# Performance work log

Hardware: AMD Instinct MI355X
Metric: run time of the kernel (lower is better)

The kernel has to match this reference:

```python
import jax, jax.numpy as jnp
import numpy as np

N_NODES = 50000
N_EDGES = 800000
F_IN = 128
HID = 64
N_LAYERS = 3
N_GRAPHS = 64
N_CLASS = 2


def setup_inputs() -> dict:
    key = jax.random.key(0)
    ks = jax.random.split(key, 8)
    x = jax.random.normal(ks[0], (N_NODES, F_IN), jnp.float32)
    edge_index = jax.random.randint(ks[1], (2, N_EDGES), 0, N_NODES, dtype=jnp.int32)
    # sorted, balanced graph assignment so every graph id appears (max-pool safe)
    batch = (jnp.arange(N_NODES, dtype=jnp.int32) * N_GRAPHS) // N_NODES

    def lin(k, fi, fo):
        return jax.random.normal(k, (fi, fo), jnp.float32) / np.sqrt(fi).astype(np.float32)

    W1 = lin(ks[2], F_IN, HID)
    W2 = lin(ks[3], HID, HID)
    W3 = lin(ks[4], HID, HID)
    lin1_W = lin(ks[5], 3 * N_LAYERS * HID, HID)
    lin2_W = lin(ks[6], HID, N_CLASS)
    return dict(
        x=x,
        W1=W1, b1=jnp.zeros((HID,), jnp.float32),
        W2=W2, b2=jnp.zeros((HID,), jnp.float32),
        W3=W3, b3=jnp.zeros((HID,), jnp.float32),
        lin1_W=lin1_W, lin1_b=jnp.zeros((HID,), jnp.float32),
        lin2_W=lin2_W, lin2_b=jnp.zeros((N_CLASS,), jnp.float32),
        edge_index=edge_index, batch=batch,
    )


def reference(x, W1, b1, W2, b2, W3, b3, lin1_W, lin1_b, lin2_W, lin2_b,
              edge_index, batch):
    src, dst = edge_index[0], edge_index[1]
    # GCN symmetric normalization with self-loops (computed once, shared by layers)
    deg = jax.ops.segment_sum(jnp.ones((N_EDGES,), jnp.float32), dst, N_NODES) + 1.0
    dinv = jax.lax.rsqrt(deg)                      # [N]
    enorm = dinv[src] * dinv[dst]                  # [E]
    self_norm = (dinv * dinv)[:, None]             # [N,1] self-loop coeff

    def gcn_conv(h, W, b):
        h = h @ W                                  # [N, HID]
        agg = jax.ops.segment_sum(h[src] * enorm[:, None], dst, N_NODES)
        return agg + self_norm * h + b

    h = jax.nn.relu(gcn_conv(x, W1, b1))
    xs = [h]
    for W, b in ((W2, b2), (W3, b3)):
        h = jax.nn.relu(gcn_conv(h, W, b))
        xs.append(h)
    hcat = jnp.concatenate(xs, axis=1)             # JK 'cat': [N, 3*HID]

    add = jax.ops.segment_sum(hcat, batch, N_GRAPHS)
    cnt = jax.ops.segment_sum(jnp.ones((N_NODES,), jnp.float32), batch, N_GRAPHS)
    mean = add / cnt[:, None]
    mx = jax.ops.segment_max(hcat, batch, N_GRAPHS)
    g = jnp.concatenate([add, mean, mx], axis=1)   # [G, 9*HID]

    g = jax.nn.relu(g @ lin1_W + lin1_b)
    # dropout p=0.5 is identity in eval mode
    logits = g @ lin2_W + lin2_b
    return jax.nn.log_softmax(logits, axis=-1)
```

## Files before the change

### kernel.cpp

```cpp
#include <hip/hip_runtime.h>
#include <hip/hip_fp16.h>

#define N_NODES 50000
#define N_EDGES 800000
#define F_IN 128
#define HID 64
#define N_GRAPHS 64

#define SCAN_B ((N_NODES + 255) / 256)
#define FUSE_B ((N_EDGES + 255) / 256)

typedef _Float16 half8 __attribute__((ext_vector_type(8)));
typedef float f32x4 __attribute__((ext_vector_type(4)));

__global__ void deg_pack(const int* __restrict__ ei, int* __restrict__ ideg, int E,
                         const float* __restrict__ W1, const float* __restrict__ W2,
                         const float* __restrict__ W3,
                         __half* __restrict__ W1t, __half* __restrict__ W2t,
                         __half* __restrict__ W3t) {
    int i = blockIdx.x * blockDim.x + threadIdx.x;
    if (i * 4 < E) {
        int4 d = ((const int4*)(ei + E))[i];
        atomicAdd(&ideg[d.x], 1);
        atomicAdd(&ideg[d.y], 1);
        atomicAdd(&ideg[d.z], 1);
        atomicAdd(&ideg[d.w], 1);
    }
    if (i < 8192) {
        int f = i >> 7, k = i & 127;
        W1t[i] = __float2half(W1[k * 64 + f]);
    } else if (i < 12288) {
        int j = i - 8192;
        int f = j >> 6, k = j & 63;
        W2t[j] = __float2half(W2[k * 64 + f]);
    } else if (i < 16384) {
        int l = i - 12288;
        int f = l >> 6, k = l & 63;
        W3t[l] = __float2half(W3[k * 64 + f]);
    }
}

__global__ void scan_part(const int* __restrict__ ideg, int* __restrict__ bsum,
                          float* __restrict__ padd, unsigned int* __restrict__ pmax,
                          int* __restrict__ pcnt, int n) {
    __shared__ int s[256];
    int t = threadIdx.x;
    if (blockIdx.x < 48) {
        int z = blockIdx.x * 256 + t;
        padd[z] = 0.f;
        pmax[z] = 0u;
        if (z < 64) pcnt[z] = 0;
    }
    int i = blockIdx.x * 256 + t;
    s[t] = (i < n) ? ideg[i] : 0;
    __syncthreads();
    for (int o = 128; o > 0; o >>= 1) {
        if (t < o) s[t] += s[t + o];
        __syncthreads();
    }
    if (t == 0) bsum[blockIdx.x] = s[0];
}

__global__ void scan_final(const int* __restrict__ ideg, const int* __restrict__ bsum,
                           int* __restrict__ offs, int* __restrict__ cur,
                           float* __restrict__ dinv, int n) {
    __shared__ int s[256];
    __shared__ int sb[256];
    int t = threadIdx.x;
    int i = blockIdx.x * 256 + t;
    int v = (i < n) ? ideg[i] : 0;
    s[t] = v;
    sb[t] = (t < SCAN_B) ? bsum[t] : 0;
    __syncthreads();
    for (int o = 1; o < 256; o <<= 1) {
        int u  = (t >= o) ? s[t - o] : 0;
        int ub = (t >= o) ? sb[t - o] : 0;
        __syncthreads();
        s[t] += u; sb[t] += ub;
        __syncthreads();
    }
    int base = (blockIdx.x == 0) ? 0 : sb[blockIdx.x - 1];
    int excl = base + s[t] - v;
    if (i < n) {
        offs[i] = excl; cur[i] = excl;
        dinv[i] = rsqrtf((float)v + 1.0f);
    }
    if (i == n - 1) offs[n] = excl + v;
}

__global__ __launch_bounds__(256) void fused_fill_mm1(
        const int* __restrict__ ei, const float* __restrict__ dinv,
        int* __restrict__ cur, unsigned int* __restrict__ csr,
        const float* __restrict__ X, const __half* __restrict__ W1t,
        __half* __restrict__ Y16, int E) {
    constexpr int SX = 136;
    __shared__ __half sXh[16 * SX];
    int tid = threadIdx.x;

    int e = blockIdx.x * 256 + tid;
    int esrc = ei[e];
    int d = ei[E + e];
    __half hw = __float2half(dinv[esrc]);
    unsigned int pk = ((unsigned int)(*(unsigned short*)&hw) << 16)
                    | (unsigned int)(esrc & 0xFFFF);
    int pos = atomicAdd(&cur[d], 1);

    int lane = tid & 63;
    int r = lane & 15, h = lane >> 4;
    int w = tid >> 6;
    const half8* Brow = (const half8*)(W1t + (size_t)(w * 16 + r) * F_IN + h * 8);
    half8 b0 = Brow[0];
    half8 b1 = Brow[4];
    half8 b2 = Brow[8];
    half8 b3 = Brow[12];

    int nodeBase = blockIdx.x * 16;
#pragma unroll
    for (int p = tid; p < 512; p += 256) {
        int row = p >> 5, c4 = p & 31;
        float4 v = *(const float4*)(X + (size_t)(nodeBase + row) * F_IN + c4 * 4);
        __half2 ab = __floats2half2_rn(v.x, v.y);
        __half2 cd = __floats2half2_rn(v.z, v.w);
        uint2 u; u.x = *(unsigned int*)&ab; u.y = *(unsigned int*)&cd;
        *(uint2*)&sXh[row * SX + c4 * 4] = u;
    }
    __syncthreads();

    f32x4 acc = {0.f, 0.f, 0.f, 0.f};
    half8 a0 = *(const half8*)&sXh[r * SX +  0 + h * 8];
    half8 a1 = *(const half8*)&sXh[r * SX + 32 + h * 8];
    half8 a2 = *(const half8*)&sXh[r * SX + 64 + h * 8];
    half8 a3 = *(const half8*)&sXh[r * SX + 96 + h * 8];
    acc = __builtin_amdgcn_mfma_f32_16x16x32_f16(a0, b0, acc, 0, 0, 0);
    acc = __builtin_amdgcn_mfma_f32_16x16x32_f16(a1, b1, acc, 0, 0, 0);
    acc = __builtin_amdgcn_mfma_f32_16x16x32_f16(a2, b2, acc, 0, 0, 0);
    acc = __builtin_amdgcn_mfma_f32_16x16x32_f16(a3, b3, acc, 0, 0, 0);
    int nodeT = nodeBase + h * 4;
#pragma unroll
    for (int reg = 0; reg < 4; ++reg)
        Y16[(size_t)(nodeT + reg) * 64 + w * 16 + r] = __float2half(acc[reg]);

    csr[pos] = pk;
}

__global__ __launch_bounds__(256) void matmul64_h(
        const __half* __restrict__ X, const __half* __restrict__ Wt,
        __half* __restrict__ Y16, int n) {
    int tid = threadIdx.x;
    int nodeBase = blockIdx.x * 64;
    int lane = tid & 63;
    int r = lane & 15, h = lane >> 4;
    int w = tid >> 6;
    int rowA = nodeBase + w * 16 + r;
    const half8* Arow = (const half8*)(X + (size_t)rowA * 64 + h * 8);
    half8 a0 = Arow[0];
    half8 a1 = Arow[4];
#pragma unroll
    for (int ft = 0; ft < 4; ++ft) {
        const half8* Brow = (const half8*)(Wt + (size_t)(ft * 16 + r) * 64 + h * 8);
        half8 b0 = Brow[0];
        half8 b1 = Brow[4];
        f32x4 acc = {0.f, 0.f, 0.f, 0.f};
        acc = __builtin_amdgcn_mfma_f32_16x16x32_f16(a0, b0, acc, 0, 0, 0);
        acc = __builtin_amdgcn_mfma_f32_16x16x32_f16(a1, b1, acc, 0, 0, 0);
        int nodeT = nodeBase + w * 16 + h * 4;
#pragma unroll
        for (int reg = 0; reg < 4; ++reg) {
            int node = nodeT + reg;
            if (node < n) Y16[(size_t)node * 64 + ft * 16 + r] = __float2half(acc[reg]);
        }
    }
}

__global__ void agg_kernel(const __half* __restrict__ hp16, const float* __restrict__ dinv,
                           const int* __restrict__ offs, const unsigned int* __restrict__ csr,
                           const float* __restrict__ b, __half* __restrict__ hout, int n) {
    int node = blockIdx.x * 4 + (threadIdx.x >> 6);
    if (node >= n) return;
    int lane = threadIdx.x & 63;
    int g = lane >> 3;
    int sub = lane & 7;
    int beg = offs[node], end = offs[node + 1];

    float dn = dinv[node];
    uint4 sv = *(const uint4*)(hp16 + (size_t)node * 64 + sub * 8);
    float4 bA = *(const float4*)(b + sub * 8);
    float4 bB = *(const float4*)(b + sub * 8 + 4);

    float a0 = 0.f, a1 = 0.f, a2 = 0.f, a3 = 0.f;
    float a4 = 0.f, a5 = 0.f, a6 = 0.f, a7 = 0.f;
    int lim = end - 1;
#pragma unroll 1
    for (int base0 = beg; base0 < end; base0 += 32) {
        int base = base0 + g * 4;
        if (base < end) {
            unsigned int pk0 = csr[base];
            unsigned int pk1 = csr[min(base + 1, lim)];
            unsigned int pk2 = csr[min(base + 2, lim)];
            unsigned int pk3 = csr[min(base + 3, lim)];
            uint4 hv0 = *(const uint4*)(hp16 + (size_t)(pk0 & 0xFFFFu) * 64 + sub * 8);
            uint4 hv1 = *(const uint4*)(hp16 + (size_t)(pk1 & 0xFFFFu) * 64 + sub * 8);
            uint4 hv2 = *(const uint4*)(hp16 + (size_t)(pk2 & 0xFFFFu) * 64 + sub * 8);
            uint4 hv3 = *(const uint4*)(hp16 + (size_t)(pk3 & 0xFFFFu) * 64 + sub * 8);
#pragma unroll
            for (int j = 0; j < 4; ++j) {
                unsigned int pkj = (j == 0) ? pk0 : (j == 1) ? pk1 : (j == 2) ? pk2 : pk3;
                uint4 hvj = (j == 0) ? hv0 : (j == 1) ? hv1 : (j == 2) ? hv2 : hv3;
                __half_raw hr; hr.x = (unsigned short)(pkj >> 16);
                float w = (base + j < end) ? __half2float(*(__half*)&hr) : 0.f;
                float2 f01 = __half22float2(*(const __half2*)&hvj.x);
                float2 f23 = __half22float2(*(const __half2*)&hvj.y);
                float2 f45 = __half22float2(*(const __half2*)&hvj.z);
                float2 f67 = __half22float2(*(const __half2*)&hvj.w);
                a0 += f01.x * w; a1 += f01.y * w; a2 += f23.x * w; a3 += f23.y * w;
                a4 += f45.x * w; a5 += f45.y * w; a6 += f67.x * w; a7 += f67.y * w;
            }
        }
    }
#pragma unroll
    for (int m = 8; m <= 32; m <<= 1) {
        a0 += __shfl_xor(a0, m); a1 += __shfl_xor(a1, m);
        a2 += __shfl_xor(a2, m); a3 += __shfl_xor(a3, m);
        a4 += __shfl_xor(a4, m); a5 += __shfl_xor(a5, m);
        a6 += __shfl_xor(a6, m); a7 += __shfl_xor(a7, m);
    }

    float2 s01 = __half22float2(*(const __half2*)&sv.x);
    float2 s23 = __half22float2(*(const __half2*)&sv.y);
    float2 s45 = __half22float2(*(const __half2*)&sv.z);
    float2 s67 = __half22float2(*(const __half2*)&sv.w);
    float dn2 = dn * dn;
    float4 rA, rB;
    rA.x = dn * a0 + dn2 * s01.x + bA.x;  rA.x = rA.x > 0.f ? rA.x : 0.f;
    rA.y = dn * a1 + dn2 * s01.y + bA.y;  rA.y = rA.y > 0.f ? rA.y : 0.f;
    rA.z = dn * a2 + dn2 * s23.x + bA.z;  rA.z = rA.z > 0.f ? rA.z : 0.f;
    rA.w = dn * a3 + dn2 * s23.y + bA.w;  rA.w = rA.w > 0.f ? rA.w : 0.f;
    rB.x = dn * a4 + dn2 * s45.x + bB.x;  rB.x = rB.x > 0.f ? rB.x : 0.f;
    rB.y = dn * a5 + dn2 * s45.y + bB.y;  rB.y = rB.y > 0.f ? rB.y : 0.f;
    rB.z = dn * a6 + dn2 * s67.x + bB.z;  rB.z = rB.z > 0.f ? rB.z : 0.f;
    rB.w = dn * a7 + dn2 * s67.y + bB.w;  rB.w = rB.w > 0.f ? rB.w : 0.f;
    if (g == 0) {
        __half2 p0 = __floats2half2_rn(rA.x, rA.y);
        __half2 p1 = __floats2half2_rn(rA.z, rA.w);
        __half2 p2 = __floats2half2_rn(rB.x, rB.y);
        __half2 p3 = __floats2half2_rn(rB.z, rB.w);
        uint4 st;
        st.x = *(unsigned int*)&p0; st.y = *(unsigned int*)&p1;
        st.z = *(unsigned int*)&p2; st.w = *(unsigned int*)&p3;
        *(uint4*)(hout + (size_t)node * 64 + sub * 8) = st;
    }
}

__global__ __launch_bounds__(192) void pool_kernel(
        const __half* __restrict__ h1, const __half* __restrict__ h2,
        const __half* __restrict__ h3, const int* __restrict__ batch,
        float* __restrict__ padd, unsigned int* __restrict__ pmax,
        int* __restrict__ pcnt, int n, int chunk) {
    __shared__ float lsum[8][192];
    __shared__ float lmax[8][192];
    int t = threadIdx.x;
    int stream = t / 24;
    int oct = t % 24;
    int L = oct >> 3, sub = oct & 7;
    int f0 = L * 64 + sub * 8;
    const __half* src = (L == 0) ? h1 : (L == 1) ? h2 : h3;
    int start = blockIdx.x * chunk;
    int end = min(start + chunk, n);
    if (start >= end) return;
    int gtail = batch[end - 1];

    float s[8] = {0.f,0.f,0.f,0.f,0.f,0.f,0.f,0.f};
    float m[8] = {0.f,0.f,0.f,0.f,0.f,0.f,0.f,0.f};
    int cnt = 0;
    int node = start + stream;
    int gcur = (node < end) ? batch[node] : gtail;
    for (; node < end; node += 8) {
        int bg = batch[node];
        if (bg != gcur) {
#pragma unroll
            for (int j = 0; j < 8; ++j) {
                unsafeAtomicAdd(&padd[gcur * 192 + f0 + j], s[j]);
                atomicMax(&pmax[gcur * 192 + f0 + j], __float_as_uint(m[j]));
                s[j] = 0.f; m[j] = 0.f;
            }
            if (oct == 0) { atomicAdd(&pcnt[gcur], cnt); cnt = 0; }
            gcur = bg;
        }
        uint4 hv = *(const uint4*)(src + (size_t)node * 64 + sub * 8);
        const __half2* hp = (const __half2*)&hv;
#pragma unroll
        for (int q = 0; q < 4; ++q) {
            float2 f2 = __half22float2(hp[q]);
            s[2*q]   += f2.x;  m[2*q]   = fmaxf(m[2*q],   f2.x);
            s[2*q+1] += f2.y;  m[2*q+1] = fmaxf(m[2*q+1], f2.y);
        }
        if (oct == 0) ++cnt;
    }
    if (oct == 0 && cnt) atomicAdd(&pcnt[gcur], cnt);
    if (gcur != gtail) {
#pragma unroll
        for (int j = 0; j < 8; ++j) {
            unsafeAtomicAdd(&padd[gcur * 192 + f0 + j], s[j]);
            atomicMax(&pmax[gcur * 192 + f0 + j], __float_as_uint(m[j]));
            s[j] = 0.f; m[j] = 0.f;
        }
    }
#pragma unroll
    for (int j = 0; j < 8; ++j) {
        lsum[stream][f0 + j] = s[j];
        lmax[stream][f0 + j] = m[j];
    }
    __syncthreads();
    float ts = 0.f, tm = 0.f;
#pragma unroll
    for (int st = 0; st < 8; ++st) {
        ts += lsum[st][t];
        tm = fmaxf(tm, lmax[st][t]);
    }
    unsafeAtomicAdd(&padd[gtail * 192 + t], ts);
    atomicMax(&pmax[gtail * 192 + t], __float_as_uint(tm));
}

__global__ void mlp_kernel(const float* __restrict__ padd, const unsigned int* __restrict__ pmax,
                           const int* __restrict__ pcnt,
                           const float* __restrict__ lin1_W, const float* __restrict__ lin1_b,
                           const float* __restrict__ lin2_W, const float* __restrict__ lin2_b,
                           float* __restrict__ out) {
    int g = blockIdx.x;
    int t = threadIdx.x;
    __shared__ float gv[576];
    __shared__ float hid[64];
    float cnt = (float)pcnt[g];
    for (int i = t; i < 192; i += 64) {
        float a = padd[g * 192 + i];
        gv[i] = a;
        gv[192 + i] = a / cnt;
        gv[384 + i] = __uint_as_float(pmax[g * 192 + i]);
    }
    __syncthreads();
    float acc = lin1_b[t];
#pragma unroll 8
    for (int k = 0; k < 576; ++k) acc += gv[k] * lin1_W[k * 64 + t];
    hid[t] = acc > 0.0f ? acc : 0.0f;
    __syncthreads();
    if (t == 0) {
        float l0 = lin2_b[0], l1 = lin2_b[1];
        for (int k = 0; k < 64; ++k) {
            l0 += hid[k] * lin2_W[k * 2 + 0];
            l1 += hid[k] * lin2_W[k * 2 + 1];
        }
        float m = fmaxf(l0, l1);
        float lse = m + logf(expf(l0 - m) + expf(l1 - m));
        out[g * 2 + 0] = l0 - lse;
        out[g * 2 + 1] = l1 - lse;
    }
}

extern "C" void kernel_launch(void* const* d_in, const int* in_sizes, int n_in,
                              void* d_out, int out_size, void* d_ws, size_t ws_size,
                              hipStream_t stream) {
    const float* x      = (const float*)d_in[0];
    const float* W1     = (const float*)d_in[1];
    const float* b1     = (const float*)d_in[2];
    const float* W2     = (const float*)d_in[3];
    const float* b2     = (const float*)d_in[4];
    const float* W3     = (const float*)d_in[5];
    const float* b3     = (const float*)d_in[6];
    const float* lin1_W = (const float*)d_in[7];
    const float* lin1_b = (const float*)d_in[8];
    const float* lin2_W = (const float*)d_in[9];
    const float* lin2_b = (const float*)d_in[10];
    const int*   ei     = (const int*)d_in[11];
    const int*   batch  = (const int*)d_in[12];
    float* out = (float*)d_out;

    char* ws = (char*)d_ws;
    size_t off = 0;
    auto alloc = [&](size_t bytes) {
        void* p = ws + off;
        off = (off + bytes + 255) & ~(size_t)255;
        return p;
    };
    int*   ideg    = (int*)  alloc(N_NODES * 4);
    float* dinv    = (float*)alloc(N_NODES * 4);
    int*   offs    = (int*)  alloc((N_NODES + 1) * 4);
    int*   cur     = (int*)  alloc(N_NODES * 4);
    int*   bsum    = (int*)  alloc(SCAN_B * 4);
    unsigned int* csr = (unsigned int*)alloc((size_t)N_EDGES * 4);
    __half* P      = (__half*)alloc((size_t)N_NODES * 64 * 2);
    __half* h1     = (__half*)alloc((size_t)N_NODES * 64 * 2);
    __half* h2     = (__half*)alloc((size_t)N_NODES * 64 * 2);
    __half* h3     = (__half*)alloc((size_t)N_NODES * 64 * 2);
    __half* W1t    = (__half*)alloc(64 * 128 * 2);
    __half* W2t    = (__half*)alloc(64 * 64 * 2);
    __half* W3t    = (__half*)alloc(64 * 64 * 2);
    float* padd    = (float*)alloc(N_GRAPHS * 192 * 4);
    unsigned int* pmax = (unsigned int*)alloc(N_GRAPHS * 192 * 4);
    int*   pcnt    = (int*) alloc(N_GRAPHS * 4);

    hipMemsetAsync(ideg, 0, N_NODES * 4, stream);
    deg_pack<<<(N_EDGES / 4 + 255) / 256, 256, 0, stream>>>(ei, ideg, N_EDGES,
                                                            W1, W2, W3, W1t, W2t, W3t);
    scan_part <<<SCAN_B, 256, 0, stream>>>(ideg, bsum, padd, pmax, pcnt, N_NODES);
    scan_final<<<SCAN_B, 256, 0, stream>>>(ideg, bsum, offs, cur, dinv, N_NODES);

    const int mmGrid  = (N_NODES + 63) / 64;
    const int aggGrid = (N_NODES + 3) / 4;

    fused_fill_mm1<<<FUSE_B, 256, 0, stream>>>(ei, dinv, cur, csr, x, W1t, P, N_EDGES);
    agg_kernel<<<aggGrid, 256, 0, stream>>>(P, dinv, offs, csr, b1, h1, N_NODES);
    matmul64_h<<<mmGrid, 256, 0, stream>>>(h1, W2t, P, N_NODES);
    agg_kernel<<<aggGrid, 256, 0, stream>>>(P, dinv, offs, csr, b2, h2, N_NODES);
    matmul64_h<<<mmGrid, 256, 0, stream>>>(h2, W3t, P, N_NODES);
    agg_kernel<<<aggGrid, 256, 0, stream>>>(P, dinv, offs, csr, b3, h3, N_NODES);

    const int chunk = (N_NODES + 511) / 512;
    pool_kernel<<<512, 192, 0, stream>>>(h1, h2, h3, batch, padd, pmax, pcnt, N_NODES, chunk);
    mlp_kernel<<<N_GRAPHS, 64, 0, stream>>>(padd, pmax, pcnt, lin1_W, lin1_b, lin2_W, lin2_b, out);
}
```

Measured before the change: 319.2 us.

## Fold source-side normalization into matmul output and shrink CSR to 16-bit indices

Each matmul epilogue now scales its output rows by dinv, so the aggregation sums unweighted neighbour rows. The per-edge weight no longer has to be stored in the CSR, which shrinks to 16-bit source indices and halves the index traffic read in each of the three aggregation passes. It also drops the dinv gather in the fill kernel. The self-loop term becomes dn*(agg+self), which is algebraically equivalent. The fp16 intermediate is now pre-scaled, which slightly changes rounding. The matmul reads dinv as float4 past N_NODES in its last block, and the 16-bit index truncation was already present.

```diff
diff --git a/kernel.cpp b/kernel.cpp
--- a/kernel.cpp
+++ b/kernel.cpp
@@ -90,7 +90,7 @@
 
 __global__ __launch_bounds__(256) void fused_fill_mm1(
         const int* __restrict__ ei, const float* __restrict__ dinv,
-        int* __restrict__ cur, unsigned int* __restrict__ csr,
+        int* __restrict__ cur, unsigned short* __restrict__ csr,
         const float* __restrict__ X, const __half* __restrict__ W1t,
         __half* __restrict__ Y16, int E) {
     constexpr int SX = 136;
@@ -98,11 +98,8 @@
     int tid = threadIdx.x;
 
     int e = blockIdx.x * 256 + tid;
-    int esrc = ei[e];
+    unsigned short srcu = (unsigned short)(ei[e] & 0xFFFF);
     int d = ei[E + e];
-    __half hw = __float2half(dinv[esrc]);
-    unsigned int pk = ((unsigned int)(*(unsigned short*)&hw) << 16)
-                    | (unsigned int)(esrc & 0xFFFF);
     int pos = atomicAdd(&cur[d], 1);
 
     int lane = tid & 63;
@@ -136,16 +133,18 @@
     acc = __builtin_amdgcn_mfma_f32_16x16x32_f16(a2, b2, acc, 0, 0, 0);
     acc = __builtin_amdgcn_mfma_f32_16x16x32_f16(a3, b3, acc, 0, 0, 0);
     int nodeT = nodeBase + h * 4;
+    float4 dv = *(const float4*)(dinv + nodeT);
+    acc[0] *= dv.x; acc[1] *= dv.y; acc[2] *= dv.z; acc[3] *= dv.w;
 #pragma unroll
     for (int reg = 0; reg < 4; ++reg)
         Y16[(size_t)(nodeT + reg) * 64 + w * 16 + r] = __float2half(acc[reg]);
 
-    csr[pos] = pk;
+    csr[pos] = srcu;
 }
 
 __global__ __launch_bounds__(256) void matmul64_h(
         const __half* __restrict__ X, const __half* __restrict__ Wt,
-        __half* __restrict__ Y16, int n) {
+        const float* __restrict__ dinv, __half* __restrict__ Y16, int n) {
     int tid = threadIdx.x;
     int nodeBase = blockIdx.x * 64;
     int lane = tid & 63;
@@ -155,6 +154,8 @@
     const half8* Arow = (const half8*)(X + (size_t)rowA * 64 + h * 8);
     half8 a0 = Arow[0];
     half8 a1 = Arow[4];
+    int nodeT = nodeBase + w * 16 + h * 4;
+    float4 dv = *(const float4*)(dinv + nodeT);
 #pragma unroll
     for (int ft = 0; ft < 4; ++ft) {
         const half8* Brow = (const half8*)(Wt + (size_t)(ft * 16 + r) * 64 + h * 8);
@@ -163,7 +164,7 @@
         f32x4 acc = {0.f, 0.f, 0.f, 0.f};
         acc = __builtin_amdgcn_mfma_f32_16x16x32_f16(a0, b0, acc, 0, 0, 0);
         acc = __builtin_amdgcn_mfma_f32_16x16x32_f16(a1, b1, acc, 0, 0, 0);
-        int nodeT = nodeBase + w * 16 + h * 4;
+        acc[0] *= dv.x; acc[1] *= dv.y; acc[2] *= dv.z; acc[3] *= dv.w;
 #pragma unroll
         for (int reg = 0; reg < 4; ++reg) {
             int node = nodeT + reg;
@@ -173,7 +174,7 @@
 }
 
 __global__ void agg_kernel(const __half* __restrict__ hp16, const float* __restrict__ dinv,
-                           const int* __restrict__ offs, const unsigned int* __restrict__ csr,
+                           const int* __restrict__ offs, const unsigned short* __restrict__ csr,
                            const float* __restrict__ b, __half* __restrict__ hout, int n) {
     int node = blockIdx.x * 4 + (threadIdx.x >> 6);
     if (node >= n) return;
@@ -194,20 +195,16 @@
     for (int base0 = beg; base0 < end; base0 += 32) {
         int base = base0 + g * 4;
         if (base < end) {
-            unsigned int pk0 = csr[base];
-            unsigned int pk1 = csr[min(base + 1, lim)];
-            unsigned int pk2 = csr[min(base + 2, lim)];
-            unsigned int pk3 = csr[min(base + 3, lim)];
-            uint4 hv0 = *(const uint4*)(hp16 + (size_t)(pk0 & 0xFFFFu) * 64 + sub * 8);
-            uint4 hv1 = *(const uint4*)(hp16 + (size_t)(pk1 & 0xFFFFu) * 64 + sub * 8);
-            uint4 hv2 = *(const uint4*)(hp16 + (size_t)(pk2 & 0xFFFFu) * 64 + sub * 8);
-            uint4 hv3 = *(const uint4*)(hp16 + (size_t)(pk3 & 0xFFFFu) * 64 + sub * 8);
+            int i0 = base, i1 = min(base + 1, lim), i2 = min(base + 2, lim), i3 = min(base + 3, lim);
+            unsigned short s0 = csr[i0], s1 = csr[i1], s2 = csr[i2], s3 = csr[i3];
+            uint4 hv0 = *(const uint4*)(hp16 + (size_t)s0 * 64 + sub * 8);
+            uint4 hv1 = *(const uint4*)(hp16 + (size_t)s1 * 64 + sub * 8);
+            uint4 hv2 = *(const uint4*)(hp16 + (size_t)s2 * 64 + sub * 8);
+            uint4 hv3 = *(const uint4*)(hp16 + (size_t)s3 * 64 + sub * 8);
 #pragma unroll
             for (int j = 0; j < 4; ++j) {
-                unsigned int pkj = (j == 0) ? pk0 : (j == 1) ? pk1 : (j == 2) ? pk2 : pk3;
                 uint4 hvj = (j == 0) ? hv0 : (j == 1) ? hv1 : (j == 2) ? hv2 : hv3;
-                __half_raw hr; hr.x = (unsigned short)(pkj >> 16);
-                float w = (base + j < end) ? __half2float(*(__half*)&hr) : 0.f;
+                float w = (base + j < end) ? 1.f : 0.f;
                 float2 f01 = __half22float2(*(const __half2*)&hvj.x);
                 float2 f23 = __half22float2(*(const __half2*)&hvj.y);
                 float2 f45 = __half22float2(*(const __half2*)&hvj.z);
@@ -229,16 +226,15 @@
     float2 s23 = __half22float2(*(const __half2*)&sv.y);
     float2 s45 = __half22float2(*(const __half2*)&sv.z);
     float2 s67 = __half22float2(*(const __half2*)&sv.w);
-    float dn2 = dn * dn;
     float4 rA, rB;
-    rA.x = dn * a0 + dn2 * s01.x + bA.x;  rA.x = rA.x > 0.f ? rA.x : 0.f;
-    rA.y = dn * a1 + dn2 * s01.y + bA.y;  rA.y = rA.y > 0.f ? rA.y : 0.f;
-    rA.z = dn * a2 + dn2 * s23.x + bA.z;  rA.z = rA.z > 0.f ? rA.z : 0.f;
-    rA.w = dn * a3 + dn2 * s23.y + bA.w;  rA.w = rA.w > 0.f ? rA.w : 0.f;
-    rB.x = dn * a4 + dn2 * s45.x + bB.x;  rB.x = rB.x > 0.f ? rB.x : 0.f;
-    rB.y = dn * a5 + dn2 * s45.y + bB.y;  rB.y = rB.y > 0.f ? rB.y : 0.f;
-    rB.z = dn * a6 + dn2 * s67.x + bB.z;  rB.z = rB.z > 0.f ? rB.z : 0.f;
-    rB.w = dn * a7 + dn2 * s67.y + bB.w;  rB.w = rB.w > 0.f ? rB.w : 0.f;
+    rA.x = dn * (a0 + s01.x) + bA.x;  rA.x = rA.x > 0.f ? rA.x : 0.f;
+    rA.y = dn * (a1 + s01.y) + bA.y;  rA.y = rA.y > 0.f ? rA.y : 0.f;
+    rA.z = dn * (a2 + s23.x) + bA.z;  rA.z = rA.z > 0.f ? rA.z : 0.f;
+    rA.w = dn * (a3 + s23.y) + bA.w;  rA.w = rA.w > 0.f ? rA.w : 0.f;
+    rB.x = dn * (a4 + s45.x) + bB.x;  rB.x = rB.x > 0.f ? rB.x : 0.f;
+    rB.y = dn * (a5 + s45.y) + bB.y;  rB.y = rB.y > 0.f ? rB.y : 0.f;
+    rB.z = dn * (a6 + s67.x) + bB.z;  rB.z = rB.z > 0.f ? rB.z : 0.f;
+    rB.w = dn * (a7 + s67.y) + bB.w;  rB.w = rB.w > 0.f ? rB.w : 0.f;
     if (g == 0) {
         __half2 p0 = __floats2half2_rn(rA.x, rA.y);
         __half2 p1 = __floats2half2_rn(rA.z, rA.w);
@@ -386,7 +382,7 @@
     int*   offs    = (int*)  alloc((N_NODES + 1) * 4);
     int*   cur     = (int*)  alloc(N_NODES * 4);
     int*   bsum    = (int*)  alloc(SCAN_B * 4);
-    unsigned int* csr = (unsigned int*)alloc((size_t)N_EDGES * 4);
+    unsigned short* csr = (unsigned short*)alloc((size_t)N_EDGES * 2);
     __half* P      = (__half*)alloc((size_t)N_NODES * 64 * 2);
     __half* h1     = (__half*)alloc((size_t)N_NODES * 64 * 2);
     __half* h2     = (__half*)alloc((size_t)N_NODES * 64 * 2);
@@ -409,9 +405,9 @@
 
     fused_fill_mm1<<<FUSE_B, 256, 0, stream>>>(ei, dinv, cur, csr, x, W1t, P, N_EDGES);
     agg_kernel<<<aggGrid, 256, 0, stream>>>(P, dinv, offs, csr, b1, h1, N_NODES);
-    matmul64_h<<<mmGrid, 256, 0, stream>>>(h1, W2t, P, N_NODES);
+    matmul64_h<<<mmGrid, 256, 0, stream>>>(h1, W2t, dinv, P, N_NODES);
     agg_kernel<<<aggGrid, 256, 0, stream>>>(P, dinv, offs, csr, b2, h2, N_NODES);
-    matmul64_h<<<mmGrid, 256, 0, stream>>>(h2, W3t, P, N_NODES);
+    matmul64_h<<<mmGrid, 256, 0, stream>>>(h2, W3t, dinv, P, N_NODES);
     agg_kernel<<<aggGrid, 256, 0, stream>>>(P, dinv, offs, csr, b3, h3, N_NODES);
 
     const int chunk = (N_NODES + 511) / 512;
```

After: 319.9 us. About the same (+0.2%).
